# Performance work log

Hardware: AMD Instinct MI355X
Metric: run time of the kernel (lower is better)

The kernel has to match this reference:

```python
import jax, jax.numpy as jnp
import numpy as np

EPS = 1e-5


def _conv3x3(x, w):
    # x: [B,C,H,W], w: [O,I,3,3], stride 1, padding 1
    return jax.lax.conv_general_dilated(
        x, w, window_strides=(1, 1), padding=((1, 1), (1, 1)),
        dimension_numbers=("NCHW", "OIHW", "NCHW"))


def _bn(x, g, b, m, v):
    # inference-mode BatchNorm2d over channel dim
    inv = jax.lax.rsqrt(v + EPS) * g
    return x * inv[None, :, None, None] + (b - m * inv)[None, :, None, None]


def setup_inputs() -> dict:
    key = jax.random.key(0)
    B, C, H, W = 32, 256, 56, 56
    ks = jax.random.split(key, 16)
    x = jax.random.normal(ks[0], (B, C, H, W), dtype=jnp.float32)
    mask = (jax.random.uniform(ks[1], (B, 1, H, W)) < 0.5).astype(jnp.float32)
    # dilated mask = 3x3 max-pool of mask
    mask_dilate = jax.lax.reduce_window(
        mask, -jnp.inf, jax.lax.max, (1, 1, 3, 3), (1, 1, 1, 1), "SAME")
    mask_dilate = jnp.maximum(mask_dilate, 0.0).astype(jnp.float32)
    vector = (jax.random.uniform(ks[2], (B, C)) < 0.5).astype(jnp.float32)
    conv1_w = jax.random.normal(ks[3], (C, C, 3, 3), dtype=jnp.float32) * 0.05
    conv2_w = jax.random.normal(ks[4], (C, C, 3, 3), dtype=jnp.float32) * 0.05
    bn1_g = 1.0 + 0.1 * jax.random.normal(ks[5], (C,), dtype=jnp.float32)
    bn1_b = 0.1 * jax.random.normal(ks[6], (C,), dtype=jnp.float32)
    bn1_m = 0.1 * jax.random.normal(ks[7], (C,), dtype=jnp.float32)
    bn1_v = 0.5 + jax.random.uniform(ks[8], (C,), dtype=jnp.float32)
    bn2_g = 1.0 + 0.1 * jax.random.normal(ks[9], (C,), dtype=jnp.float32)
    bn2_b = 0.1 * jax.random.normal(ks[10], (C,), dtype=jnp.float32)
    bn2_m = 0.1 * jax.random.normal(ks[11], (C,), dtype=jnp.float32)
    bn2_v = 0.5 + jax.random.uniform(ks[12], (C,), dtype=jnp.float32)
    return dict(x=x, mask=mask, mask_dilate=mask_dilate, vector=vector,
                conv1_w=conv1_w, bn1_g=bn1_g, bn1_b=bn1_b, bn1_m=bn1_m, bn1_v=bn1_v,
                conv2_w=conv2_w, bn2_g=bn2_g, bn2_b=bn2_b, bn2_m=bn2_m, bn2_v=bn2_v)


def reference(x, mask, mask_dilate, vector,
              conv1_w, bn1_g, bn1_b, bn1_m, bn1_v,
              conv2_w, bn2_g, bn2_b, bn2_m, bn2_v):
    # Sparse BasicBlock, stride=1, no downsample, input_mask=True.
    identity = x
    h = x * mask_dilate                      # apply_mask(x, mask_dilate)
    h = _conv3x3(h, conv1_w) * mask          # conv3x3_mask(conv1, ...)
    h = jax.nn.relu(_bn(h, bn1_g, bn1_b, bn1_m, bn1_v)) * mask_dilate  # bn_relu_mask(bn1, relu, ., mask_dilate)
    h = h * mask                             # apply_mask(x, mask)
    h = h * vector[:, :, None, None]         # channel_process(x, vector)
    h = _conv3x3(h, conv2_w) * mask          # conv3x3_mask(conv2, ...)
    h = _bn(h, bn2_g, bn2_b, bn2_m, bn2_v) * mask  # bn_relu_mask(bn2, None, ., mask)
    out = identity + h * mask                # identity + apply_mask(x, mask)
    return jax.nn.relu(out)
```

## Files before the change

kernel.cpp:

```cpp
#include <hip/hip_runtime.h>
#include <cstdint>


#define EPS 1e-5f

constexpr int Bn = 32, Cc = 256, Hh = 56, Ww = 56;
constexpr int HW = Hh * Ww;
constexpr int PD = 58;
constexpr int PP = PD * PD;
constexpr int WP_ELEMS = 2 * 16 * 9 * 2 * 128 * 8;

typedef __bf16 bf16x8 __attribute__((ext_vector_type(8)));
typedef float  f32x16 __attribute__((ext_vector_type(16)));

__global__ void pack_xm(const float* __restrict__ x, const float* __restrict__ md,
                        __bf16* __restrict__ xm) {
    int prow = blockIdx.x, img = blockIdx.y;
    int gy = prow - 1;
    bool rv = (unsigned)gy < 56u;
    size_t rowbase = ((size_t)img * PD + prow) * PD * Cc;
    for (int u = threadIdx.x; u < 32 * 64; u += 256) {
        int cg = u >> 6, pcol = u & 63;
        if (pcol >= PD) continue;
        int gx = pcol - 1;
        bf16x8 v = {};
        if (rv && (unsigned)gx < 56u) {
            float mdv = md[img * HW + gy * 56 + gx];
            const float* xp = x + ((size_t)img * Cc + cg * 8) * HW + gy * 56 + gx;
            #pragma unroll
            for (int j = 0; j < 8; ++j)
                v[j] = (__bf16)(xp[(size_t)j * HW] * mdv);
        }
        *(bf16x8*)&xm[rowbase + (size_t)pcol * Cc + cg * 8] = v;
    }
}

__global__ void zero_u_halo(__bf16* __restrict__ u) {
    int img = blockIdx.x;
    __bf16* base = u + (size_t)img * PP * Cc;
    bf16x8 z = {};
    for (int t = threadIdx.x; t < 228 * 32; t += 256) {
        int site = t >> 5, cg = (t & 31) * 8;
        int prow, pcol;
        if (site < 58)       { prow = 0;          pcol = site; }
        else if (site < 116) { prow = 57;         pcol = site - 58; }
        else if (site < 172) { prow = site - 115; pcol = 0; }
        else                 { prow = site - 171; pcol = 57; }
        *(bf16x8*)&base[((size_t)prow * PD + pcol) * Cc + cg] = z;
    }
}

__global__ void pack_w(const float* __restrict__ w1, const float* __restrict__ w2,
                       __bf16* __restrict__ wp1, __bf16* __restrict__ wp2) {
    int id = blockIdx.x * 256 + threadIdx.x;
    const float* w = blockIdx.y ? w2 : w1;
    __bf16* wp = blockIdx.y ? wp2 : wp1;
    int j = id & 7; int t = id >> 3;
    int col = t & 127; t >>= 7;
    int half = t & 1; t >>= 1;
    int tap = t % 9; t /= 9;
    int chunk = t & 15; int coblk = t >> 4;
    int co = coblk * 128 + col;
    int ci = chunk * 16 + half * 8 + j;
    wp[id] = (__bf16)(w[((size_t)co * Cc + ci) * 9 + tap]);
}

__global__ void bn_prep(const float* g1, const float* b1, const float* m1, const float* v1,
                        const float* g2, const float* b2, const float* m2, const float* v2,
                        float* binv1, float* bbeta1, float* binv2, float* bbeta2) {
    int c = threadIdx.x;
    float i1 = g1[c] * rsqrtf(v1[c] + EPS);
    binv1[c] = i1; bbeta1[c] = b1[c] - m1[c] * i1;
    float i2 = g2[c] * rsqrtf(v2[c] + EPS);
    binv2[c] = i2; bbeta2[c] = b2[c] - m2[c] * i2;
}

__device__ __forceinline__ void gl_lds16(const __bf16* g, __bf16* l) {
    __builtin_amdgcn_global_load_lds(
        (const __attribute__((address_space(1))) void*)g,
        (__attribute__((address_space(3))) void*)l, 16, 0, 0);
}

template <bool C1>
__global__ __launch_bounds__(512, 2)
void conv_kern(const __bf16* __restrict__ src,
               const __bf16* __restrict__ wp,
               const float* __restrict__ maskg,
               const float* __restrict__ vec,
               const float* __restrict__ binv, const float* __restrict__ bbeta,
               const float* __restrict__ xin,
               void* __restrict__ dstv) {
    constexpr int SIN1 = 2 * 10 * 66 * 8;
    constexpr int SW1  = 9 * 2 * 128 * 8;
    __shared__ __align__(16) __bf16 s_in[2 * SIN1];
    __shared__ __align__(16) __bf16 s_w[2 * SW1];

    const int tid = threadIdx.x;
    const int lane = tid & 63, wave = tid >> 6;
    const int xlane = lane & 31, halfid = lane >> 5;
    const int pxw = wave >> 1, cow = wave & 1;

    const int bid = blockIdx.x;
    const int wg = (bid & 7) * 56 + (bid >> 3);
    const int img = wg / 14;
    const int t = wg - img * 14;
    const int y0 = (t >> 1) * 8;
    const int coblk = t & 1;
    const int co0c = coblk * 128;

    f32x16 acc[4][2];
    #pragma unroll
    for (int a = 0; a < 4; ++a)
        #pragma unroll
        for (int b = 0; b < 2; ++b)
            #pragma unroll
            for (int r = 0; r < 16; ++r) acc[a][b][r] = 0.f;

    const __bf16* wblk = wp + (size_t)coblk * (16 * SW1);
    const float* maskp = maskg + (size_t)img * HW;
    const __bf16* srcimg = src + (size_t)img * PP * Cc;

    auto STAGE = [&](int b, int chunk) {
        for (int u0 = wave * 64; u0 < 1320; u0 += 512) {
            int u = u0 + lane;
            if (u < 1320) {
                int half = u / 660, rem = u - half * 660;
                int row = rem / 66, xx = rem - row * 66;
                int pcol = xx < PD ? xx : PD - 1;
                const __bf16* g = srcimg + ((size_t)((y0 + row) * PD + pcol)) * Cc +
                                  chunk * 16 + half * 8;
                gl_lds16(g, &s_in[b * SIN1 + u0 * 8]);
            }
        }
        const __bf16* g = wblk + (size_t)chunk * SW1;
        for (int u0 = wave * 64; u0 < 2304; u0 += 512)
            gl_lds16(g + (size_t)(u0 + lane) * 8, &s_w[b * SW1 + u0 * 8]);
    };

    STAGE(0, 0);
    asm volatile("s_waitcnt vmcnt(0)" ::: "memory");
    __builtin_amdgcn_s_barrier();
    __builtin_amdgcn_sched_barrier(0);

    for (int c = 0; c < 16; ++c) {
        const int b = c & 1;
        if (c < 15) STAGE(b ^ 1, c + 1);
        const int sib = b * SIN1, swb = b * SW1;

        __builtin_amdgcn_s_setprio(1);
        #pragma unroll
        for (int kh = 0; kh < 3; ++kh)
            #pragma unroll
            for (int kw = 0; kw < 3; ++kw) {
                const int tap = kh * 3 + kw;
                bf16x8 wf[2], inf[4];
                #pragma unroll
                for (int jt = 0; jt < 2; ++jt)
                    wf[jt] = *(const bf16x8*)&s_w[swb + ((tap * 2 + halfid) * 128 +
                                                   (cow * 2 + jt) * 32 + xlane) * 8];
                #pragma unroll
                for (int it = 0; it < 4; ++it) {
                    int tg = pxw * 4 + it;
                    int yy = (tg >> 1) + kh;
                    int xx = (tg & 1) * 32 + xlane + kw;
                    inf[it] = *(const bf16x8*)&s_in[sib + ((halfid * 10 + yy) * 66 + xx) * 8];
                }
                #pragma unroll
                for (int it = 0; it < 4; ++it)
                    #pragma unroll
                    for (int jt = 0; jt < 2; ++jt) {
                        if constexpr (C1)
                            acc[it][jt] = __builtin_amdgcn_mfma_f32_32x32x16_bf16(
                                inf[it], wf[jt], acc[it][jt], 0, 0, 0);
                        else
                            acc[it][jt] = __builtin_amdgcn_mfma_f32_32x32x16_bf16(
                                wf[jt], inf[it], acc[it][jt], 0, 0, 0);
                    }
            }
        __builtin_amdgcn_s_setprio(0);
        __builtin_amdgcn_sched_barrier(0);
        asm volatile("s_waitcnt vmcnt(0)" ::: "memory");
        __builtin_amdgcn_s_barrier();
        __builtin_amdgcn_sched_barrier(0);
    }

    if constexpr (C1) {
        __bf16* u = (__bf16*)dstv;
        float iv[2], bt[2], vv[2]; int cog[2];
        #pragma unroll
        for (int jt = 0; jt < 2; ++jt) {
            cog[jt] = co0c + (cow * 2 + jt) * 32 + xlane;
            iv[jt] = binv[cog[jt]];
            bt[jt] = bbeta[cog[jt]];
            vv[jt] = vec[img * Cc + cog[jt]];
        }
        #pragma unroll
        for (int it = 0; it < 4; ++it) {
            int tg = pxw * 4 + it;
            int y = y0 + (tg >> 1), xb = (tg & 1) * 32;
            #pragma unroll
            for (int reg = 0; reg < 16; ++reg) {
                int x = xb + (reg & 3) + 8 * (reg >> 2) + 4 * halfid;
                if (x < 56) {
                    float mv = maskp[y * 56 + x];
                    size_t base = ((size_t)(img * PD + y + 1) * PD + (x + 1)) * Cc;
                    #pragma unroll
                    for (int jt = 0; jt < 2; ++jt) {
                        float o = fmaxf(fmaf(acc[it][jt][reg], iv[jt], bt[jt]), 0.f)
                                  * mv * vv[jt];
                        u[base + cog[jt]] = (__bf16)o;
                    }
                }
            }
        }
    } else {
        float* outp = (float*)dstv;
        int ya[4], xa[4]; float mva[4]; bool ok[4];
        #pragma unroll
        for (int it = 0; it < 4; ++it) {
            int tg = pxw * 4 + it;
            ya[it] = y0 + (tg >> 1);
            xa[it] = (tg & 1) * 32 + xlane;
            ok[it] = xa[it] < 56;
            mva[it] = ok[it] ? maskp[ya[it] * 56 + xa[it]] : 0.f;
        }
        #pragma unroll
        for (int jt = 0; jt < 2; ++jt) {
            int cb = co0c + (cow * 2 + jt) * 32;
            #pragma unroll
            for (int rg = 0; rg < 4; ++rg) {
                int c4 = cb + 8 * rg + 4 * halfid;
                float4 iv4 = *(const float4*)&binv[c4];
                float4 bt4 = *(const float4*)&bbeta[c4];
                float ivv[4] = {iv4.x, iv4.y, iv4.z, iv4.w};
                float btv[4] = {bt4.x, bt4.y, bt4.z, bt4.w};
                #pragma unroll
                for (int j = 0; j < 4; ++j) {
                    int reg = rg * 4 + j;
                    int co = c4 + j;
                    size_t cbase = (size_t)(img * Cc + co) * HW;
                    #pragma unroll
                    for (int it = 0; it < 4; ++it) {
                        if (ok[it]) {
                            size_t oa = cbase + ya[it] * 56 + xa[it];
                            float o = fmaxf(
                                xin[oa] + mva[it] * fmaf(acc[it][jt][reg], ivv[j], btv[j]),
                                0.f);
                            outp[oa] = o;
                        }
                    }
                }
            }
        }
    }
}

extern "C" void kernel_launch(void* const* d_in, const int* in_sizes, int n_in,
                              void* d_out, int out_size, void* d_ws, size_t ws_size,
                              hipStream_t stream) {
    const float* x    = (const float*)d_in[0];
    const float* mask = (const float*)d_in[1];
    const float* md   = (const float*)d_in[2];
    const float* vec  = (const float*)d_in[3];
    const float* w1   = (const float*)d_in[4];
    const float* bn1g = (const float*)d_in[5];
    const float* bn1b = (const float*)d_in[6];
    const float* bn1m = (const float*)d_in[7];
    const float* bn1v = (const float*)d_in[8];
    const float* w2   = (const float*)d_in[9];
    const float* bn2g = (const float*)d_in[10];
    const float* bn2b = (const float*)d_in[11];
    const float* bn2m = (const float*)d_in[12];
    const float* bn2v = (const float*)d_in[13];
    float* out = (float*)d_out;

    const size_t npad = (size_t)Bn * PP * Cc;
    __bf16* xm  = (__bf16*)d_ws;
    __bf16* u   = xm + npad;
    __bf16* wp1 = u + npad;
    __bf16* wp2 = wp1 + WP_ELEMS;
    float* binv1  = (float*)(wp2 + WP_ELEMS);
    float* bbeta1 = binv1 + 256;
    float* binv2  = bbeta1 + 256;
    float* bbeta2 = binv2 + 256;

    pack_xm<<<dim3(PD, Bn), dim3(256), 0, stream>>>(x, md, xm);
    zero_u_halo<<<dim3(Bn), dim3(256), 0, stream>>>(u);
    pack_w<<<dim3(WP_ELEMS / 256, 2), dim3(256), 0, stream>>>(w1, w2, wp1, wp2);
    bn_prep<<<dim3(1), dim3(256), 0, stream>>>(bn1g, bn1b, bn1m, bn1v,
                                               bn2g, bn2b, bn2m, bn2v,
                                               binv1, bbeta1, binv2, bbeta2);

    conv_kern<true><<<dim3(448), dim3(512), 0, stream>>>(
        xm, wp1, mask, vec, binv1, bbeta1, nullptr, u);
    conv_kern<false><<<dim3(448), dim3(512), 0, stream>>>(
        u, wp2, mask, nullptr, binv2, bbeta2, x, out);
}
```

Before: 593.5 us.

## Triple-buffer input tiles and split conv main loop into staged kh phases

```diff
diff --git a/kernel.cpp b/kernel.cpp
--- a/kernel.cpp
+++ b/kernel.cpp
@@ -81,6 +81,48 @@
         (__attribute__((address_space(3))) void*)l, 16, 0, 0);
 }
 
+#define PHASE(G, STAGE_STMT)                                                    \
+    {                                                                           \
+        bf16x8 wf[3][2], inf[3][4];                                             \
+        _Pragma("unroll")                                                       \
+        for (int tt = 0; tt < 3; ++tt) {                                        \
+            const int tap = (G) * 3 + tt;                                       \
+            _Pragma("unroll")                                                   \
+            for (int jt = 0; jt < 2; ++jt)                                      \
+                wf[tt][jt] = *(const bf16x8*)&sw[((tap * 2 + halfid) * 128 +    \
+                                            (cow * 2 + jt) * 32 + xlane) * 8];  \
+            _Pragma("unroll")                                                   \
+            for (int it = 0; it < 4; ++it) {                                    \
+                int tg = pxw * 4 + it;                                          \
+                int yy = (tg >> 1) + (G);                                       \
+                int xx = (tg & 1) * 32 + xlane + tt;                            \
+                inf[tt][it] = *(const bf16x8*)&si[((halfid * 10 + yy) * 66 + xx) * 8]; \
+            }                                                                   \
+        }                                                                       \
+        STAGE_STMT;                                                             \
+        __builtin_amdgcn_sched_barrier(0);                                      \
+        __builtin_amdgcn_s_barrier();                                           \
+        asm volatile("s_waitcnt lgkmcnt(0)" ::: "memory");                      \
+        __builtin_amdgcn_sched_barrier(0);                                      \
+        __builtin_amdgcn_s_setprio(1);                                          \
+        _Pragma("unroll")                                                       \
+        for (int tt = 0; tt < 3; ++tt)                                          \
+            _Pragma("unroll")                                                   \
+            for (int it = 0; it < 4; ++it)                                      \
+                _Pragma("unroll")                                               \
+                for (int jt = 0; jt < 2; ++jt) {                                \
+                    if constexpr (C1)                                           \
+                        acc[it][jt] = __builtin_amdgcn_mfma_f32_32x32x16_bf16(  \
+                            inf[tt][it], wf[tt][jt], acc[it][jt], 0, 0, 0);     \
+                    else                                                        \
+                        acc[it][jt] = __builtin_amdgcn_mfma_f32_32x32x16_bf16(  \
+                            wf[tt][jt], inf[tt][it], acc[it][jt], 0, 0, 0);     \
+                }                                                               \
+        __builtin_amdgcn_s_setprio(0);                                          \
+        __builtin_amdgcn_sched_barrier(0);                                      \
+        __builtin_amdgcn_s_barrier();                                           \
+    }
+
 template <bool C1>
 __global__ __launch_bounds__(512, 2)
 void conv_kern(const __bf16* __restrict__ src,
@@ -90,10 +132,10 @@
                const float* __restrict__ binv, const float* __restrict__ bbeta,
                const float* __restrict__ xin,
                void* __restrict__ dstv) {
-    constexpr int SIN1 = 2 * 10 * 66 * 8;
-    constexpr int SW1  = 9 * 2 * 128 * 8;
-    __shared__ __align__(16) __bf16 s_in[2 * SIN1];
-    __shared__ __align__(16) __bf16 s_w[2 * SW1];
+    constexpr int SINB = 2 * 10 * 66 * 8;
+    constexpr int SWB  = 9 * 2 * 128 * 8;
+    __shared__ __align__(16) __bf16 s_in[3 * SINB];
+    __shared__ __align__(16) __bf16 s_w[2 * SWB];
 
     const int tid = threadIdx.x;
     const int lane = tid & 63, wave = tid >> 6;
@@ -116,72 +158,60 @@
             #pragma unroll
             for (int r = 0; r < 16; ++r) acc[a][b][r] = 0.f;
 
-    const __bf16* wblk = wp + (size_t)coblk * (16 * SW1);
+    const __bf16* wblk = wp + (size_t)coblk * (16 * SWB);
     const float* maskp = maskg + (size_t)img * HW;
     const __bf16* srcimg = src + (size_t)img * PP * Cc;
 
-    auto STAGE = [&](int b, int chunk) {
-        for (int u0 = wave * 64; u0 < 1320; u0 += 512) {
+    auto STAGE_IN = [&](int buf, int chunk) {
+        const int base = wave * 165;
+        #pragma unroll
+        for (int k = 0; k < 3; ++k) {
+            int u0 = base + k * 64;
             int u = u0 + lane;
-            if (u < 1320) {
+            if (u < base + 165) {
                 int half = u / 660, rem = u - half * 660;
                 int row = rem / 66, xx = rem - row * 66;
                 int pcol = xx < PD ? xx : PD - 1;
-                const __bf16* g = srcimg + ((size_t)((y0 + row) * PD + pcol)) * Cc +
-                                  chunk * 16 + half * 8;
-                gl_lds16(g, &s_in[b * SIN1 + u0 * 8]);
+                gl_lds16(srcimg + ((size_t)((y0 + row) * PD + pcol)) * Cc +
+                             chunk * 16 + half * 8,
+                         &s_in[buf * SINB + u0 * 8]);
             }
         }
-        const __bf16* g = wblk + (size_t)chunk * SW1;
-        for (int u0 = wave * 64; u0 < 2304; u0 += 512)
-            gl_lds16(g + (size_t)(u0 + lane) * 8, &s_w[b * SW1 + u0 * 8]);
     };
-
-    STAGE(0, 0);
-    asm volatile("s_waitcnt vmcnt(0)" ::: "memory");
+    auto STAGE_W = [&](int buf, int chunk) {
+        const __bf16* g = wblk + (size_t)chunk * SWB;
+        const int base = wave * 288;
+        #pragma unroll
+        for (int k = 0; k < 5; ++k) {
+            int u0 = base + k * 64;
+            int u = u0 + lane;
+            if (u < base + 288)
+                gl_lds16(g + (size_t)u * 8, &s_w[buf * SWB + u0 * 8]);
+        }
+    };
+
+    STAGE_W(0, 0);
+    STAGE_IN(0, 0);
+    STAGE_IN(1, 1);
+    asm volatile("s_waitcnt vmcnt(3)" ::: "memory");
     __builtin_amdgcn_s_barrier();
     __builtin_amdgcn_sched_barrier(0);
 
     for (int c = 0; c < 16; ++c) {
-        const int b = c & 1;
-        if (c < 15) STAGE(b ^ 1, c + 1);
-        const int sib = b * SIN1, swb = b * SW1;
-
-        __builtin_amdgcn_s_setprio(1);
-        #pragma unroll
-        for (int kh = 0; kh < 3; ++kh)
-            #pragma unroll
-            for (int kw = 0; kw < 3; ++kw) {
-                const int tap = kh * 3 + kw;
-                bf16x8 wf[2], inf[4];
-                #pragma unroll
-                for (int jt = 0; jt < 2; ++jt)
-                    wf[jt] = *(const bf16x8*)&s_w[swb + ((tap * 2 + halfid) * 128 +
-                                                   (cow * 2 + jt) * 32 + xlane) * 8];
-                #pragma unroll
-                for (int it = 0; it < 4; ++it) {
-                    int tg = pxw * 4 + it;
-                    int yy = (tg >> 1) + kh;
-                    int xx = (tg & 1) * 32 + xlane + kw;
-                    inf[it] = *(const bf16x8*)&s_in[sib + ((halfid * 10 + yy) * 66 + xx) * 8];
-                }
-                #pragma unroll
-                for (int it = 0; it < 4; ++it)
-                    #pragma unroll
-                    for (int jt = 0; jt < 2; ++jt) {
-                        if constexpr (C1)
-                            acc[it][jt] = __builtin_amdgcn_mfma_f32_32x32x16_bf16(
-                                inf[it], wf[jt], acc[it][jt], 0, 0, 0);
-                        else
-                            acc[it][jt] = __builtin_amdgcn_mfma_f32_32x32x16_bf16(
-                                wf[jt], inf[it], acc[it][jt], 0, 0, 0);
-                    }
-            }
-        __builtin_amdgcn_s_setprio(0);
-        __builtin_amdgcn_sched_barrier(0);
-        asm volatile("s_waitcnt vmcnt(0)" ::: "memory");
-        __builtin_amdgcn_s_barrier();
-        __builtin_amdgcn_sched_barrier(0);
+        const __bf16* si = &s_in[(c % 3) * SINB];
+        const __bf16* sw = &s_w[(c & 1) * SWB];
+
+        PHASE(0, { if (c < 15) STAGE_W((c + 1) & 1, c + 1); });
+        PHASE(1, { if (c < 14) STAGE_IN((c + 2) % 3, c + 2); });
+        PHASE(2, { });
+
+        if (c < 15) {
+            if (c < 14) asm volatile("s_waitcnt vmcnt(3)" ::: "memory");
+            else        asm volatile("s_waitcnt vmcnt(0)" ::: "memory");
+            __builtin_amdgcn_sched_barrier(0);
+            __builtin_amdgcn_s_barrier();
+            __builtin_amdgcn_sched_barrier(0);
+        }
     }
 
     if constexpr (C1) {
```

After: 697.1 us. 17.5% more time.

## Store padded activations as channel-group slabs and split per-wave staging loops

Applied to the files above, without the earlier changes.

```diff
diff --git a/kernel.cpp b/kernel.cpp
--- a/kernel.cpp
+++ b/kernel.cpp
@@ -7,7 +7,8 @@
 constexpr int Bn = 32, Cc = 256, Hh = 56, Ww = 56;
 constexpr int HW = Hh * Ww;
 constexpr int PD = 58;
-constexpr int PP = PD * PD;
+constexpr int SLAB = PD * PD * 8;
+constexpr int IMG_ELEMS = 16 * 2 * SLAB;
 constexpr int WP_ELEMS = 2 * 16 * 9 * 2 * 128 * 8;
 
 typedef __bf16 bf16x8 __attribute__((ext_vector_type(8)));
@@ -18,7 +19,6 @@
     int prow = blockIdx.x, img = blockIdx.y;
     int gy = prow - 1;
     bool rv = (unsigned)gy < 56u;
-    size_t rowbase = ((size_t)img * PD + prow) * PD * Cc;
     for (int u = threadIdx.x; u < 32 * 64; u += 256) {
         int cg = u >> 6, pcol = u & 63;
         if (pcol >= PD) continue;
@@ -31,22 +31,22 @@
             for (int j = 0; j < 8; ++j)
                 v[j] = (__bf16)(xp[(size_t)j * HW] * mdv);
         }
-        *(bf16x8*)&xm[rowbase + (size_t)pcol * Cc + cg * 8] = v;
+        *(bf16x8*)&xm[(size_t)(img * 32 + cg) * SLAB + (prow * PD + pcol) * 8] = v;
     }
 }
 
 __global__ void zero_u_halo(__bf16* __restrict__ u) {
     int img = blockIdx.x;
-    __bf16* base = u + (size_t)img * PP * Cc;
+    __bf16* base = u + (size_t)img * IMG_ELEMS;
     bf16x8 z = {};
-    for (int t = threadIdx.x; t < 228 * 32; t += 256) {
-        int site = t >> 5, cg = (t & 31) * 8;
+    for (int t = threadIdx.x; t < 32 * 228; t += 256) {
+        int slab = t / 228, site = t - slab * 228;
         int prow, pcol;
         if (site < 58)       { prow = 0;          pcol = site; }
         else if (site < 116) { prow = 57;         pcol = site - 58; }
         else if (site < 172) { prow = site - 115; pcol = 0; }
         else                 { prow = site - 171; pcol = 57; }
-        *(bf16x8*)&base[((size_t)prow * PD + pcol) * Cc + cg] = z;
+        *(bf16x8*)&base[(size_t)slab * SLAB + (prow * PD + pcol) * 8] = z;
     }
 }
 
@@ -90,10 +90,10 @@
                const float* __restrict__ binv, const float* __restrict__ bbeta,
                const float* __restrict__ xin,
                void* __restrict__ dstv) {
-    constexpr int SIN1 = 2 * 10 * 66 * 8;
-    constexpr int SW1  = 9 * 2 * 128 * 8;
-    __shared__ __align__(16) __bf16 s_in[2 * SIN1];
-    __shared__ __align__(16) __bf16 s_w[2 * SW1];
+    constexpr int SINB = 2 * 10 * 66 * 8;
+    constexpr int SWB  = 9 * 2 * 128 * 8;
+    __shared__ __align__(16) __bf16 s_in[2 * SINB];
+    __shared__ __align__(16) __bf16 s_w[2 * SWB];
 
     const int tid = threadIdx.x;
     const int lane = tid & 63, wave = tid >> 6;
@@ -116,36 +116,49 @@
             #pragma unroll
             for (int r = 0; r < 16; ++r) acc[a][b][r] = 0.f;
 
-    const __bf16* wblk = wp + (size_t)coblk * (16 * SW1);
+    const __bf16* wblk = wp + (size_t)coblk * (16 * SWB);
     const float* maskp = maskg + (size_t)img * HW;
-    const __bf16* srcimg = src + (size_t)img * PP * Cc;
-
-    auto STAGE = [&](int b, int chunk) {
-        for (int u0 = wave * 64; u0 < 1320; u0 += 512) {
+    const __bf16* srcimg = src + (size_t)img * IMG_ELEMS;
+
+    auto STAGE_IN = [&](int buf, int chunk) {
+        const __bf16* slab = srcimg + (size_t)chunk * (2 * SLAB);
+        const int base = wave * 165;
+        #pragma unroll
+        for (int k = 0; k < 3; ++k) {
+            int u0 = base + k * 64;
             int u = u0 + lane;
-            if (u < 1320) {
+            if (u < base + 165) {
                 int half = u / 660, rem = u - half * 660;
                 int row = rem / 66, xx = rem - row * 66;
                 int pcol = xx < PD ? xx : PD - 1;
-                const __bf16* g = srcimg + ((size_t)((y0 + row) * PD + pcol)) * Cc +
-                                  chunk * 16 + half * 8;
-                gl_lds16(g, &s_in[b * SIN1 + u0 * 8]);
+                gl_lds16(slab + ((size_t)half * SLAB) +
+                             ((y0 + row) * PD + pcol) * 8,
+                         &s_in[buf * SINB + u0 * 8]);
             }
         }
-        const __bf16* g = wblk + (size_t)chunk * SW1;
-        for (int u0 = wave * 64; u0 < 2304; u0 += 512)
-            gl_lds16(g + (size_t)(u0 + lane) * 8, &s_w[b * SW1 + u0 * 8]);
     };
-
-    STAGE(0, 0);
+    auto STAGE_W = [&](int buf, int chunk) {
+        const __bf16* g = wblk + (size_t)chunk * SWB;
+        const int base = wave * 288;
+        #pragma unroll
+        for (int k = 0; k < 5; ++k) {
+            int u0 = base + k * 64;
+            int u = u0 + lane;
+            if (u < base + 288)
+                gl_lds16(g + (size_t)u * 8, &s_w[buf * SWB + u0 * 8]);
+        }
+    };
+
+    STAGE_W(0, 0);
+    STAGE_IN(0, 0);
     asm volatile("s_waitcnt vmcnt(0)" ::: "memory");
     __builtin_amdgcn_s_barrier();
     __builtin_amdgcn_sched_barrier(0);
 
     for (int c = 0; c < 16; ++c) {
         const int b = c & 1;
-        if (c < 15) STAGE(b ^ 1, c + 1);
-        const int sib = b * SIN1, swb = b * SW1;
+        if (c < 15) { STAGE_W(b ^ 1, c + 1); STAGE_IN(b ^ 1, c + 1); }
+        const int sib = b * SINB, swb = b * SWB;
 
         __builtin_amdgcn_s_setprio(1);
         #pragma unroll
@@ -186,13 +199,14 @@
 
     if constexpr (C1) {
         __bf16* u = (__bf16*)dstv;
-        float iv[2], bt[2], vv[2]; int cog[2];
+        float iv[2], bt[2], vv[2]; int cog[2]; size_t slb[2];
         #pragma unroll
         for (int jt = 0; jt < 2; ++jt) {
             cog[jt] = co0c + (cow * 2 + jt) * 32 + xlane;
             iv[jt] = binv[cog[jt]];
             bt[jt] = bbeta[cog[jt]];
             vv[jt] = vec[img * Cc + cog[jt]];
+            slb[jt] = (size_t)(img * 32 + (cog[jt] >> 3)) * SLAB + (cog[jt] & 7);
         }
         #pragma unroll
         for (int it = 0; it < 4; ++it) {
@@ -203,12 +217,12 @@
                 int x = xb + (reg & 3) + 8 * (reg >> 2) + 4 * halfid;
                 if (x < 56) {
                     float mv = maskp[y * 56 + x];
-                    size_t base = ((size_t)(img * PD + y + 1) * PD + (x + 1)) * Cc;
+                    int poff = ((y + 1) * PD + (x + 1)) * 8;
                     #pragma unroll
                     for (int jt = 0; jt < 2; ++jt) {
                         float o = fmaxf(fmaf(acc[it][jt][reg], iv[jt], bt[jt]), 0.f)
                                   * mv * vv[jt];
-                        u[base + cog[jt]] = (__bf16)o;
+                        u[slb[jt] + poff] = (__bf16)o;
                     }
                 }
             }
@@ -274,7 +288,7 @@
     const float* bn2v = (const float*)d_in[13];
     float* out = (float*)d_out;
 
-    const size_t npad = (size_t)Bn * PP * Cc;
+    const size_t npad = (size_t)Bn * IMG_ELEMS;
     __bf16* xm  = (__bf16*)d_ws;
     __bf16* u   = xm + npad;
     __bf16* wp1 = u + npad;
```

After: 546.4 us. 7.9% less time.
